# Kernel optimization log

Hardware: AMD Instinct MI355X
Metric: run time of the kernel (lower is better)

## Reference

```python
import jax, jax.numpy as jnp
import numpy as np

N1, E1 = 500_000, 4_000_000   # g_list[1]: path-complex graph
N0, E0 = 200_000, 1_000_000   # g_list[0]; E0 == 2*N1 (repeat-by-2 glue)
D_RBF = 64
GAMMA = 0.1


def rbf_map(x, W, b):
    # sklearn RBFSampler random Fourier features: sqrt(2/D) * cos(x @ W + b)
    return jnp.sqrt(2.0 / D_RBF) * jnp.cos(x @ W + b)


def gat_conv(x, W, al, ar, b, src, dst, num_nodes):
    # DGL GATConv: gather -> LeakyReLU edge attention -> per-dst softmax -> scatter-sum
    H, F = al.shape
    h = (x @ W).reshape(-1, H, F)                 # [N, H, F]
    el = jnp.sum(h * al, axis=-1)                 # [N, H]
    er = jnp.sum(h * ar, axis=-1)                 # [N, H]
    e = jax.nn.leaky_relu(el[src] + er[dst], 0.2) # [E, H]
    emax = jax.ops.segment_max(e, dst, num_segments=num_nodes)
    emax = jnp.where(jnp.isfinite(emax), emax, 0.0)
    a = jnp.exp(e - emax[dst])                    # [E, H]
    denom = jax.ops.segment_sum(a, dst, num_segments=num_nodes)          # [N, H]
    num = jax.ops.segment_sum(a[:, :, None] * h[src], dst, num_segments=num_nodes)  # [N, H, F]
    return num / jnp.maximum(denom, 1e-9)[:, :, None] + b.reshape(1, H, F)


def setup_inputs() -> dict:
    key = jax.random.key(0)
    ks = jax.random.split(key, 32)
    s = 0.1
    inp = {
        'feat1': jax.random.normal(ks[0], (N1, 2), jnp.float32),
        'src1': jax.random.randint(ks[1], (E1,), 0, N1, jnp.int32),
        'dst1': jax.random.randint(ks[2], (E1,), 0, N1, jnp.int32),
        'feat0': jax.random.normal(ks[3], (N0, 62), jnp.float32),
        'src0': jax.random.randint(ks[4], (E0,), 0, N0, jnp.int32),
        'dst0': jax.random.randint(ks[5], (E0,), 0, N0, jnp.int32),
        'edge_feat0': jax.random.normal(ks[6], (E0, 1), jnp.float32),
        'W_rbf1': jax.random.normal(ks[7], (2, D_RBF), jnp.float32) * np.sqrt(2.0 * GAMMA),
        'b_rbf1': jax.random.uniform(ks[8], (D_RBF,), jnp.float32) * (2.0 * np.pi),
        'W_rbf0': jax.random.normal(ks[9], (62, D_RBF), jnp.float32) * np.sqrt(2.0 * GAMMA),
        'b_rbf0': jax.random.uniform(ks[10], (D_RBF,), jnp.float32) * (2.0 * np.pi),
        'g1c1_W': jax.random.normal(ks[11], (64, 16), jnp.float32) * s,
        'g1c1_al': jax.random.normal(ks[12], (2, 8), jnp.float32) * s,
        'g1c1_ar': jax.random.normal(ks[13], (2, 8), jnp.float32) * s,
        'g1c1_b': jnp.zeros((16,), jnp.float32),
        'g1c2_W': jax.random.normal(ks[14], (16, 1), jnp.float32) * s,
        'g1c2_al': jax.random.normal(ks[15], (1, 1), jnp.float32) * s,
        'g1c2_ar': jax.random.normal(ks[16], (1, 1), jnp.float32) * s,
        'g1c2_b': jnp.zeros((1,), jnp.float32),
        'g2c1_W': jax.random.normal(ks[17], (64, 16), jnp.float32) * s,
        'g2c1_al': jax.random.normal(ks[18], (2, 8), jnp.float32) * s,
        'g2c1_ar': jax.random.normal(ks[19], (2, 8), jnp.float32) * s,
        'g2c1_b': jnp.zeros((16,), jnp.float32),
        'g2c2_W': jax.random.normal(ks[20], (16, 64), jnp.float32) * s,
        'g2c2_al': jax.random.normal(ks[21], (1, 64), jnp.float32) * s,
        'g2c2_ar': jax.random.normal(ks[22], (1, 64), jnp.float32) * s,
        'g2c2_b': jnp.zeros((64,), jnp.float32),
        'fc1_w': jax.random.normal(ks[23], (16, 64), jnp.float32) * s,
        'fc1_b': jnp.zeros((16,), jnp.float32),
        'out_w': jax.random.normal(ks[24], (1, 16), jnp.float32) * s,
        'out_b': jnp.zeros((1,), jnp.float32),
    }
    return inp


def reference(feat1, src1, dst1, feat0, src0, dst0, edge_feat0,
              W_rbf1, b_rbf1, W_rbf0, b_rbf0,
              g1c1_W, g1c1_al, g1c1_ar, g1c1_b,
              g1c2_W, g1c2_al, g1c2_ar, g1c2_b,
              g2c1_W, g2c1_al, g2c1_ar, g2c1_b,
              g2c2_W, g2c2_al, g2c2_ar, g2c2_b,
              fc1_w, fc1_b, out_w, out_b):
    # ---- branch on g_list[1] ----
    nf1 = rbf_map(feat1, W_rbf1, b_rbf1)                                  # [N1, 64]
    h1 = gat_conv(nf1, g1c1_W, g1c1_al, g1c1_ar, g1c1_b, src1, dst1, N1).reshape(N1, 16)
    h1 = jax.nn.relu(h1)
    out1 = gat_conv(h1, g1c2_W, g1c2_al, g1c2_ar, g1c2_b, src1, dst1, N1).reshape(N1, 1)
    # repeat-each-row-twice + add g0 edge feats (dead wrt final output: GATConv
    # has no .weight attr so initialize_weights is a no-op in the original too)
    ef = jnp.repeat(out1, 2, axis=0) + edge_feat0                         # [E0, 1]
    _ = ef
    # ---- branch on g_list[0] ----
    nf0 = rbf_map(feat0, W_rbf0, b_rbf0)                                  # [N0, 64]
    h0 = gat_conv(nf0, g2c1_W, g2c1_al, g2c1_ar, g2c1_b, src0, dst0, N0).reshape(N0, 16)
    h0 = jax.nn.relu(h0)
    out2 = gat_conv(h0, g2c2_W, g2c2_al, g2c2_ar, g2c2_b, src0, dst0, N0).reshape(N0, 64)
    # ---- dense tail ----
    h = jnp.mean(out2, axis=0, keepdims=True)                             # [1, 64]
    h = jax.nn.relu(h)                                                    # dropout: eval identity
    h = jax.nn.relu(h @ fc1_w.T + fc1_b)                                  # [1, 16]
    h = h @ out_w.T + out_b                                               # [1, 1]
    return jnp.squeeze(h, axis=1)                                         # [1]
```

## Files before the change

kernel.cpp:

```cpp
#include <hip/hip_runtime.h>
#include <math.h>


#define LRELU(v) ((v) > 0.0f ? (v) : 0.2f * (v))

__global__ __launch_bounds__(64) void k_prep(const float* __restrict__ W2,
                                             const float* __restrict__ al2,
                                             const float* __restrict__ ar2,
                                             float* __restrict__ wl,
                                             float* __restrict__ wr) {
    int i = threadIdx.x;
    if (i >= 16) return;
    float sl = 0.f, sr = 0.f;
    for (int f = 0; f < 64; ++f) {
        float w = W2[i * 64 + f];
        sl += w * al2[f];
        sr += w * ar2[f];
    }
    wl[i] = sl;
    wr[i] = sr;
}

__global__ __launch_bounds__(256) void k_rbf_proj(
    const float* __restrict__ feat0, const float* __restrict__ Wr,
    const float* __restrict__ br, const float* __restrict__ W1,
    const float* __restrict__ al1, const float* __restrict__ ar1,
    float* __restrict__ h1p, float* __restrict__ el1, float* __restrict__ er1,
    int N) {
    int n = blockIdx.x * blockDim.x + threadIdx.x;
    if (n >= N) return;

    float x[62];
    const float2* fp = reinterpret_cast<const float2*>(feat0 + (size_t)n * 62);
#pragma unroll
    for (int k = 0; k < 31; ++k) {
        float2 v = fp[k];
        x[2 * k] = v.x;
        x[2 * k + 1] = v.y;
    }

    float hp[16];
#pragma unroll
    for (int i = 0; i < 16; ++i) hp[i] = 0.f;

    const float cst = 0.17677669529663687f;
#pragma unroll 4
    for (int j = 0; j < 64; ++j) {
        float acc = br[j];
#pragma unroll
        for (int k = 0; k < 62; ++k) acc += x[k] * Wr[k * 64 + j];
        float nfj = cst * cosf(acc);
#pragma unroll
        for (int i = 0; i < 16; ++i) hp[i] += nfj * W1[j * 16 + i];
    }

    float e_l[2] = {0.f, 0.f}, e_r[2] = {0.f, 0.f};
#pragma unroll
    for (int i = 0; i < 16; ++i) {
        e_l[i >> 3] += hp[i] * al1[i];
        e_r[i >> 3] += hp[i] * ar1[i];
    }

    float4* ho = reinterpret_cast<float4*>(h1p + (size_t)n * 16);
    ho[0] = make_float4(hp[0], hp[1], hp[2], hp[3]);
    ho[1] = make_float4(hp[4], hp[5], hp[6], hp[7]);
    ho[2] = make_float4(hp[8], hp[9], hp[10], hp[11]);
    ho[3] = make_float4(hp[12], hp[13], hp[14], hp[15]);
    el1[n * 2 + 0] = e_l[0];
    el1[n * 2 + 1] = e_l[1];
    er1[n * 2 + 0] = e_r[0];
    er1[n * 2 + 1] = e_r[1];
}

__global__ __launch_bounds__(256) void k_edge1(
    const int* __restrict__ src, const int* __restrict__ dst,
    const float* __restrict__ el, const float* __restrict__ er,
    const float* __restrict__ hsrc, float* __restrict__ num,
    float* __restrict__ den, int E) {
    int tid = blockIdx.x * blockDim.x + threadIdx.x;
    int e = tid >> 4;
    if (e >= E) return;
    int t = tid & 15;
    int h = t >> 3;
    int s = src[e], d = dst[e];
    float v = el[s * 2 + h] + er[d * 2 + h];
    v = LRELU(v);
    float a = __expf(v);
    float hv = hsrc[(size_t)s * 16 + t];
    atomicAdd(&num[(size_t)d * 16 + t], a * hv);
    if ((t & 7) == 0) atomicAdd(&den[d * 2 + h], a);
}

__global__ __launch_bounds__(256) void k_fin1(
    const float* __restrict__ num, const float* __restrict__ den,
    const float* __restrict__ b1, const float* __restrict__ wl,
    const float* __restrict__ wr, float* __restrict__ h0,
    float* __restrict__ el2, float* __restrict__ er2, int N) {
    int n = blockIdx.x * blockDim.x + threadIdx.x;
    if (n >= N) return;
    float dn0 = fmaxf(den[n * 2 + 0], 1e-9f);
    float dn1 = fmaxf(den[n * 2 + 1], 1e-9f);
    const float4* np = reinterpret_cast<const float4*>(num + (size_t)n * 16);
    float q[16];
#pragma unroll
    for (int v4 = 0; v4 < 4; ++v4) {
        float4 nv = np[v4];
        q[v4 * 4 + 0] = nv.x;
        q[v4 * 4 + 1] = nv.y;
        q[v4 * 4 + 2] = nv.z;
        q[v4 * 4 + 3] = nv.w;
    }
    float sl = 0.f, sr = 0.f;
#pragma unroll
    for (int i = 0; i < 16; ++i) {
        float dn = (i < 8) ? dn0 : dn1;
        float val = q[i] / dn + b1[i];
        val = fmaxf(val, 0.f);
        q[i] = val;
        sl += val * wl[i];
        sr += val * wr[i];
    }
    float4* ho = reinterpret_cast<float4*>(h0 + (size_t)n * 16);
    ho[0] = make_float4(q[0], q[1], q[2], q[3]);
    ho[1] = make_float4(q[4], q[5], q[6], q[7]);
    ho[2] = make_float4(q[8], q[9], q[10], q[11]);
    ho[3] = make_float4(q[12], q[13], q[14], q[15]);
    el2[n] = sl;
    er2[n] = sr;
}

__global__ __launch_bounds__(256) void k_edge2(
    const int* __restrict__ src, const int* __restrict__ dst,
    const float* __restrict__ el, const float* __restrict__ er,
    const float* __restrict__ h0, float* __restrict__ num,
    float* __restrict__ den, int E) {
    int tid = blockIdx.x * blockDim.x + threadIdx.x;
    int e = tid >> 4;
    if (e >= E) return;
    int t = tid & 15;
    int s = src[e], d = dst[e];
    float v = el[s] + er[d];
    v = LRELU(v);
    float a = __expf(v);
    float hv = h0[(size_t)s * 16 + t];
    atomicAdd(&num[(size_t)d * 16 + t], a * hv);
    if (t == 0) atomicAdd(&den[d], a);
}

__global__ __launch_bounds__(256) void k_sum(const float* __restrict__ num,
                                             const float* __restrict__ den,
                                             float* __restrict__ s16, int N) {
    int tid = blockIdx.x * blockDim.x + threadIdx.x;
    int t = tid & 15;
    int g = tid >> 4;
    int ngrp = (gridDim.x * blockDim.x) >> 4;
    float acc = 0.f;
    for (int n = g; n < N; n += ngrp) {
        float dn = fmaxf(den[n], 1e-9f);
        acc += num[(size_t)n * 16 + t] / dn;
    }
    __shared__ float lds[256];
    lds[threadIdx.x] = acc;
    __syncthreads();
    if (threadIdx.x < 16) {
        float s = 0.f;
        for (int i = threadIdx.x; i < 256; i += 16) s += lds[i];
        atomicAdd(&s16[threadIdx.x], s);
    }
}

__global__ __launch_bounds__(64) void k_tail(
    const float* __restrict__ s16, const float* __restrict__ W2,
    const float* __restrict__ b2, const float* __restrict__ fc1w,
    const float* __restrict__ fc1b, const float* __restrict__ outw,
    const float* __restrict__ outb, float* __restrict__ out, float invN) {
    if (threadIdx.x != 0 || blockIdx.x != 0) return;
    float m[16];
#pragma unroll
    for (int i = 0; i < 16; ++i) m[i] = s16[i] * invN;
    float h16[16];
#pragma unroll
    for (int j = 0; j < 16; ++j) h16[j] = 0.f;
    for (int f = 0; f < 64; ++f) {
        float v = b2[f];
#pragma unroll
        for (int i = 0; i < 16; ++i) v += m[i] * W2[i * 64 + f];
        v = fmaxf(v, 0.f);
#pragma unroll
        for (int j = 0; j < 16; ++j) h16[j] += v * fc1w[j * 64 + f];
    }
    float o = outb[0];
#pragma unroll
    for (int j = 0; j < 16; ++j) {
        float t = fmaxf(h16[j] + fc1b[j], 0.f);
        o += t * outw[j];
    }
    out[0] = o;
}

extern "C" void kernel_launch(void* const* d_in, const int* in_sizes, int n_in,
                              void* d_out, int out_size, void* d_ws,
                              size_t ws_size, hipStream_t stream) {
    const float* feat0 = (const float*)d_in[3];
    const int* src0 = (const int*)d_in[4];
    const int* dst0 = (const int*)d_in[5];
    const float* Wr = (const float*)d_in[9];
    const float* br = (const float*)d_in[10];
    const float* W1 = (const float*)d_in[19];
    const float* al1 = (const float*)d_in[20];
    const float* ar1 = (const float*)d_in[21];
    const float* b1 = (const float*)d_in[22];
    const float* W2 = (const float*)d_in[23];
    const float* al2 = (const float*)d_in[24];
    const float* ar2 = (const float*)d_in[25];
    const float* b2 = (const float*)d_in[26];
    const float* fc1w = (const float*)d_in[27];
    const float* fc1b = (const float*)d_in[28];
    const float* outw = (const float*)d_in[29];
    const float* outb = (const float*)d_in[30];

    const int N = in_sizes[3] / 62;
    const int E = in_sizes[4];
    const size_t Nz = (size_t)N;

    float* ws = (float*)d_ws;
    float* num1 = ws;
    float* den1 = ws + 16 * Nz;
    float* num2 = ws + 18 * Nz;
    float* den2 = ws + 34 * Nz;
    float* s16 = ws + 35 * Nz;
    float* wl = ws + 35 * Nz + 16;
    float* wr = ws + 35 * Nz + 32;
    float* h1p = ws + 35 * Nz + 48;
    float* el1 = h1p + 16 * Nz;
    float* er1 = el1 + 2 * Nz;
    float* h0 = er1 + 2 * Nz;
    float* el2 = h0 + 16 * Nz;
    float* er2 = el2 + Nz;

    hipMemsetAsync(ws, 0, (35 * Nz + 16) * sizeof(float), stream);

    const int nb = (N + 255) / 256;
    const long long etot = (long long)E * 16;
    const int eb = (int)((etot + 255) / 256);

    k_prep<<<1, 64, 0, stream>>>(W2, al2, ar2, wl, wr);
    k_rbf_proj<<<nb, 256, 0, stream>>>(feat0, Wr, br, W1, al1, ar1, h1p, el1,
                                       er1, N);
    k_edge1<<<eb, 256, 0, stream>>>(src0, dst0, el1, er1, h1p, num1, den1, E);
    k_fin1<<<nb, 256, 0, stream>>>(num1, den1, b1, wl, wr, h0, el2, er2, N);
    k_edge2<<<eb, 256, 0, stream>>>(src0, dst0, el2, er2, h0, num2, den2, E);
    k_sum<<<256, 256, 0, stream>>>(num2, den2, s16, N);
    k_tail<<<1, 64, 0, stream>>>(s16, W2, b2, fc1w, fc1b, outw, outb,
                                 (float*)d_out, 1.0f / (float)N);
}
```

Before: 469.8 us.

## Build dst-sorted CSR on device and replace atomic edge scatter with per-node gather

Each call now builds a CSR by destination: a degree histogram, a three-kernel prefix scan and an atomic fill pass. The two GAT layers become gather kernels in which 16 lanes per destination node accumulate the numerator and denominator in registers. The finalize step and the node-mean reduction are fused into those kernels. This removes the 16 float atomics per edge and the large zeroing memset, at the cost of extra preprocessing launches and atomics on integer counters. Per-node loops now follow each node's in-degree, so work per group varies.

```diff
diff --git a/kernel.cpp b/kernel.cpp
--- a/kernel.cpp
+++ b/kernel.cpp
@@ -21,6 +21,77 @@
     wr[i] = sr;
 }
 
+__global__ __launch_bounds__(256) void k_hist(const int* __restrict__ dst,
+                                              int* __restrict__ deg, int E) {
+    int e = blockIdx.x * 256 + threadIdx.x;
+    if (e < E) atomicAdd(&deg[dst[e]], 1);
+}
+
+__global__ __launch_bounds__(1024) void k_scan1(const int* __restrict__ deg,
+                                                int* __restrict__ partial,
+                                                int N) {
+    __shared__ int lds[1024];
+    int i = blockIdx.x * 1024 + threadIdx.x;
+    lds[threadIdx.x] = (i < N) ? deg[i] : 0;
+    __syncthreads();
+    for (int s = 512; s > 0; s >>= 1) {
+        if (threadIdx.x < s) lds[threadIdx.x] += lds[threadIdx.x + s];
+        __syncthreads();
+    }
+    if (threadIdx.x == 0) partial[blockIdx.x] = lds[0];
+}
+
+__global__ __launch_bounds__(256) void k_scan2(const int* __restrict__ partial,
+                                               int* __restrict__ partoff,
+                                               int nb) {
+    __shared__ int lds[256];
+    int t = threadIdx.x;
+    int v = (t < nb) ? partial[t] : 0;
+    lds[t] = v;
+    __syncthreads();
+    for (int s = 1; s < 256; s <<= 1) {
+        int add = (t >= s) ? lds[t - s] : 0;
+        __syncthreads();
+        lds[t] += add;
+        __syncthreads();
+    }
+    if (t < nb) partoff[t] = lds[t] - v;
+}
+
+__global__ __launch_bounds__(1024) void k_scan3(const int* __restrict__ deg,
+                                                const int* __restrict__ partoff,
+                                                int* __restrict__ off,
+                                                int* __restrict__ cur, int N) {
+    __shared__ int lds[1024];
+    int t = threadIdx.x;
+    int i = blockIdx.x * 1024 + t;
+    int v = (i < N) ? deg[i] : 0;
+    lds[t] = v;
+    __syncthreads();
+    for (int s = 1; s < 1024; s <<= 1) {
+        int add = (t >= s) ? lds[t - s] : 0;
+        __syncthreads();
+        lds[t] += add;
+        __syncthreads();
+    }
+    if (i < N) {
+        int ex = lds[t] - v + partoff[blockIdx.x];
+        off[i] = ex;
+        cur[i] = ex;
+    }
+}
+
+__global__ __launch_bounds__(256) void k_fill(const int* __restrict__ src,
+                                              const int* __restrict__ dst,
+                                              int* __restrict__ cur,
+                                              int* __restrict__ csr, int E) {
+    int e = blockIdx.x * 256 + threadIdx.x;
+    if (e >= E) return;
+    int d = dst[e];
+    int pos = atomicAdd(&cur[d], 1);
+    csr[pos] = src[e];
+}
+
 __global__ __launch_bounds__(256) void k_rbf_proj(
     const float* __restrict__ feat0, const float* __restrict__ Wr,
     const float* __restrict__ br, const float* __restrict__ W1,
@@ -72,101 +143,67 @@
     er1[n * 2 + 1] = e_r[1];
 }
 
-__global__ __launch_bounds__(256) void k_edge1(
-    const int* __restrict__ src, const int* __restrict__ dst,
-    const float* __restrict__ el, const float* __restrict__ er,
-    const float* __restrict__ hsrc, float* __restrict__ num,
-    float* __restrict__ den, int E) {
-    int tid = blockIdx.x * blockDim.x + threadIdx.x;
-    int e = tid >> 4;
-    if (e >= E) return;
-    int t = tid & 15;
-    int h = t >> 3;
-    int s = src[e], d = dst[e];
-    float v = el[s * 2 + h] + er[d * 2 + h];
-    v = LRELU(v);
-    float a = __expf(v);
-    float hv = hsrc[(size_t)s * 16 + t];
-    atomicAdd(&num[(size_t)d * 16 + t], a * hv);
-    if ((t & 7) == 0) atomicAdd(&den[d * 2 + h], a);
-}
-
-__global__ __launch_bounds__(256) void k_fin1(
-    const float* __restrict__ num, const float* __restrict__ den,
+__global__ __launch_bounds__(256) void k_gat1(
+    const int* __restrict__ off, const int* __restrict__ deg,
+    const int* __restrict__ csr, const float* __restrict__ el1,
+    const float* __restrict__ er1, const float* __restrict__ h1p,
     const float* __restrict__ b1, const float* __restrict__ wl,
     const float* __restrict__ wr, float* __restrict__ h0,
     float* __restrict__ el2, float* __restrict__ er2, int N) {
-    int n = blockIdx.x * blockDim.x + threadIdx.x;
-    if (n >= N) return;
-    float dn0 = fmaxf(den[n * 2 + 0], 1e-9f);
-    float dn1 = fmaxf(den[n * 2 + 1], 1e-9f);
-    const float4* np = reinterpret_cast<const float4*>(num + (size_t)n * 16);
-    float q[16];
-#pragma unroll
-    for (int v4 = 0; v4 < 4; ++v4) {
-        float4 nv = np[v4];
-        q[v4 * 4 + 0] = nv.x;
-        q[v4 * 4 + 1] = nv.y;
-        q[v4 * 4 + 2] = nv.z;
-        q[v4 * 4 + 3] = nv.w;
-    }
-    float sl = 0.f, sr = 0.f;
-#pragma unroll
-    for (int i = 0; i < 16; ++i) {
-        float dn = (i < 8) ? dn0 : dn1;
-        float val = q[i] / dn + b1[i];
-        val = fmaxf(val, 0.f);
-        q[i] = val;
-        sl += val * wl[i];
-        sr += val * wr[i];
-    }
-    float4* ho = reinterpret_cast<float4*>(h0 + (size_t)n * 16);
-    ho[0] = make_float4(q[0], q[1], q[2], q[3]);
-    ho[1] = make_float4(q[4], q[5], q[6], q[7]);
-    ho[2] = make_float4(q[8], q[9], q[10], q[11]);
-    ho[3] = make_float4(q[12], q[13], q[14], q[15]);
-    el2[n] = sl;
-    er2[n] = sr;
-}
-
-__global__ __launch_bounds__(256) void k_edge2(
-    const int* __restrict__ src, const int* __restrict__ dst,
-    const float* __restrict__ el, const float* __restrict__ er,
-    const float* __restrict__ h0, float* __restrict__ num,
-    float* __restrict__ den, int E) {
-    int tid = blockIdx.x * blockDim.x + threadIdx.x;
-    int e = tid >> 4;
-    if (e >= E) return;
-    int t = tid & 15;
-    int s = src[e], d = dst[e];
-    float v = el[s] + er[d];
-    v = LRELU(v);
-    float a = __expf(v);
-    float hv = h0[(size_t)s * 16 + t];
-    atomicAdd(&num[(size_t)d * 16 + t], a * hv);
-    if (t == 0) atomicAdd(&den[d], a);
-}
-
-__global__ __launch_bounds__(256) void k_sum(const float* __restrict__ num,
-                                             const float* __restrict__ den,
-                                             float* __restrict__ s16, int N) {
-    int tid = blockIdx.x * blockDim.x + threadIdx.x;
-    int t = tid & 15;
-    int g = tid >> 4;
-    int ngrp = (gridDim.x * blockDim.x) >> 4;
-    float acc = 0.f;
-    for (int n = g; n < N; n += ngrp) {
-        float dn = fmaxf(den[n], 1e-9f);
-        acc += num[(size_t)n * 16 + t] / dn;
-    }
-    __shared__ float lds[256];
-    lds[threadIdx.x] = acc;
-    __syncthreads();
-    if (threadIdx.x < 16) {
-        float s = 0.f;
-        for (int i = threadIdx.x; i < 256; i += 16) s += lds[i];
-        atomicAdd(&s16[threadIdx.x], s);
-    }
+    int tid = blockIdx.x * 256 + threadIdx.x;
+    int d = tid >> 4;
+    if (d >= N) return;
+    int t = tid & 15, h = t >> 3;
+    float erd = er1[d * 2 + h];
+    int start = off[d], dg = deg[d];
+    float acc = 0.f, den = 0.f;
+    for (int j = 0; j < dg; ++j) {
+        int s = csr[start + j];
+        float a = __expf(LRELU(el1[s * 2 + h] + erd));
+        acc += a * h1p[(size_t)s * 16 + t];
+        den += a;
+    }
+    float val = fmaxf(acc / fmaxf(den, 1e-9f) + b1[t], 0.f);
+    h0[(size_t)d * 16 + t] = val;
+    float pl = val * wl[t], pr = val * wr[t];
+#pragma unroll
+    for (int m = 1; m < 16; m <<= 1) {
+        pl += __shfl_xor(pl, m);
+        pr += __shfl_xor(pr, m);
+    }
+    if (t == 0) {
+        el2[d] = pl;
+        er2[d] = pr;
+    }
+}
+
+__global__ __launch_bounds__(256) void k_gat2(
+    const int* __restrict__ off, const int* __restrict__ deg,
+    const int* __restrict__ csr, const float* __restrict__ el2,
+    const float* __restrict__ er2, const float* __restrict__ h0,
+    float* __restrict__ s16, int N) {
+    __shared__ float bsum[16];
+    if (threadIdx.x < 16) bsum[threadIdx.x] = 0.f;
+    __syncthreads();
+    int t = threadIdx.x & 15;
+    int g = (blockIdx.x * 256 + threadIdx.x) >> 4;
+    int ng = (gridDim.x * 256) >> 4;
+    float tot = 0.f;
+    for (int d = g; d < N; d += ng) {
+        float erd = er2[d];
+        int start = off[d], dg = deg[d];
+        float acc = 0.f, den = 0.f;
+        for (int j = 0; j < dg; ++j) {
+            int s = csr[start + j];
+            float a = __expf(LRELU(el2[s] + erd));
+            acc += a * h0[(size_t)s * 16 + t];
+            den += a;
+        }
+        tot += acc / fmaxf(den, 1e-9f);
+    }
+    atomicAdd(&bsum[t], tot);
+    __syncthreads();
+    if (threadIdx.x < 16) atomicAdd(&s16[threadIdx.x], bsum[threadIdx.x]);
 }
 
 __global__ __launch_bounds__(64) void k_tail(
@@ -223,34 +260,41 @@
     const int E = in_sizes[4];
     const size_t Nz = (size_t)N;
 
-    float* ws = (float*)d_ws;
-    float* num1 = ws;
-    float* den1 = ws + 16 * Nz;
-    float* num2 = ws + 18 * Nz;
-    float* den2 = ws + 34 * Nz;
-    float* s16 = ws + 35 * Nz;
-    float* wl = ws + 35 * Nz + 16;
-    float* wr = ws + 35 * Nz + 32;
-    float* h1p = ws + 35 * Nz + 48;
+    int* ws_i = (int*)d_ws;
+    float* ws_f = (float*)d_ws;
+    int* deg = ws_i;
+    float* s16 = ws_f + Nz;
+    int* off = ws_i + Nz + 16;
+    int* cur = ws_i + 2 * Nz + 16;
+    int* partial = ws_i + 3 * Nz + 16;
+    int* partoff = ws_i + 3 * Nz + 272;
+    int* csr = ws_i + 3 * Nz + 528;
+    float* h1p = ws_f + 3 * Nz + 528 + (size_t)E;
     float* el1 = h1p + 16 * Nz;
     float* er1 = el1 + 2 * Nz;
     float* h0 = er1 + 2 * Nz;
     float* el2 = h0 + 16 * Nz;
     float* er2 = el2 + Nz;
-
-    hipMemsetAsync(ws, 0, (35 * Nz + 16) * sizeof(float), stream);
-
-    const int nb = (N + 255) / 256;
-    const long long etot = (long long)E * 16;
-    const int eb = (int)((etot + 255) / 256);
+    float* wl = er2 + Nz;
+    float* wr = wl + 16;
+
+    hipMemsetAsync(deg, 0, (Nz + 16) * sizeof(float), stream);
+
+    const int nb_n = (N + 255) / 256;
+    const int nb_e = (E + 255) / 256;
+    const int nb_scan = (N + 1023) / 1024;
 
     k_prep<<<1, 64, 0, stream>>>(W2, al2, ar2, wl, wr);
-    k_rbf_proj<<<nb, 256, 0, stream>>>(feat0, Wr, br, W1, al1, ar1, h1p, el1,
-                                       er1, N);
-    k_edge1<<<eb, 256, 0, stream>>>(src0, dst0, el1, er1, h1p, num1, den1, E);
-    k_fin1<<<nb, 256, 0, stream>>>(num1, den1, b1, wl, wr, h0, el2, er2, N);
-    k_edge2<<<eb, 256, 0, stream>>>(src0, dst0, el2, er2, h0, num2, den2, E);
-    k_sum<<<256, 256, 0, stream>>>(num2, den2, s16, N);
+    k_hist<<<nb_e, 256, 0, stream>>>(dst0, deg, E);
+    k_scan1<<<nb_scan, 1024, 0, stream>>>(deg, partial, N);
+    k_scan2<<<1, 256, 0, stream>>>(partial, partoff, nb_scan);
+    k_scan3<<<nb_scan, 1024, 0, stream>>>(deg, partoff, off, cur, N);
+    k_fill<<<nb_e, 256, 0, stream>>>(src0, dst0, cur, csr, E);
+    k_rbf_proj<<<nb_n, 256, 0, stream>>>(feat0, Wr, br, W1, al1, ar1, h1p,
+                                         el1, er1, N);
+    k_gat1<<<(N * 16 + 255) / 256, 256, 0, stream>>>(
+        off, deg, csr, el1, er1, h1p, b1, wl, wr, h0, el2, er2, N);
+    k_gat2<<<1024, 256, 0, stream>>>(off, deg, csr, el2, er2, h0, s16, N);
     k_tail<<<1, 64, 0, stream>>>(s16, W2, b2, fc1w, fc1b, outw, outb,
                                  (float*)d_out, 1.0f / (float)N);
 }
```

New measurement: 473.0 us. About the same (+0.7%).

## Replace second-layer scatter with direct weighted sum and fuse zeroing into projection

Applied to the files above, without the earlier changes.

Layer two is now computed as a per-destination denominator pass followed by an edge pass. That edge pass accumulates a*h0[src]/den2[dst] straight into the 16-wide global sum, so the N×16 num2 scatter with per-element atomics and the separate k_sum reduction go away. The memset and k_prep are folded into the projection kernel, which also stages the RBF and W1 weights in LDS and splits the dot product across four accumulators. In exchange the edges are read twice and a division by den2 is done per edge, and summation order changes, which can alter floating-point results slightly.

```diff
diff --git a/kernel.cpp b/kernel.cpp
--- a/kernel.cpp
+++ b/kernel.cpp
@@ -3,31 +3,50 @@
 
 
 #define LRELU(v) ((v) > 0.0f ? (v) : 0.2f * (v))
-
-__global__ __launch_bounds__(64) void k_prep(const float* __restrict__ W2,
-                                             const float* __restrict__ al2,
-                                             const float* __restrict__ ar2,
-                                             float* __restrict__ wl,
-                                             float* __restrict__ wr) {
-    int i = threadIdx.x;
-    if (i >= 16) return;
-    float sl = 0.f, sr = 0.f;
-    for (int f = 0; f < 64; ++f) {
-        float w = W2[i * 64 + f];
-        sl += w * al2[f];
-        sr += w * ar2[f];
-    }
-    wl[i] = sl;
-    wr[i] = sr;
-}
 
 __global__ __launch_bounds__(256) void k_rbf_proj(
     const float* __restrict__ feat0, const float* __restrict__ Wr,
     const float* __restrict__ br, const float* __restrict__ W1,
     const float* __restrict__ al1, const float* __restrict__ ar1,
+    const float* __restrict__ W2, const float* __restrict__ al2,
+    const float* __restrict__ ar2, float* __restrict__ num1,
+    float* __restrict__ den1, float* __restrict__ den2,
+    float* __restrict__ s16, float* __restrict__ wl, float* __restrict__ wr,
     float* __restrict__ h1p, float* __restrict__ el1, float* __restrict__ er1,
     int N) {
-    int n = blockIdx.x * blockDim.x + threadIdx.x;
+    __shared__ float sWr[62 * 64];
+    __shared__ float sW1[64 * 16];
+    __shared__ float sbr[64];
+    __shared__ float sal[16], sar[16];
+
+    const int tid = threadIdx.x;
+    const int n = blockIdx.x * 256 + tid;
+
+    if (n < N) {
+        float4 z4 = make_float4(0.f, 0.f, 0.f, 0.f);
+        float4* np = reinterpret_cast<float4*>(num1 + (size_t)n * 16);
+        np[0] = z4; np[1] = z4; np[2] = z4; np[3] = z4;
+        *reinterpret_cast<float2*>(den1 + n * 2) = make_float2(0.f, 0.f);
+        den2[n] = 0.f;
+    }
+    if (blockIdx.x == 0 && tid < 16) {
+        s16[tid] = 0.f;
+        float sl = 0.f, sr = 0.f;
+        for (int f = 0; f < 64; ++f) {
+            float w = W2[tid * 64 + f];
+            sl += w * al2[f];
+            sr += w * ar2[f];
+        }
+        wl[tid] = sl;
+        wr[tid] = sr;
+    }
+
+    for (int i = tid; i < 62 * 64; i += 256) sWr[i] = Wr[i];
+    for (int i = tid; i < 64 * 16; i += 256) sW1[i] = W1[i];
+    if (tid < 64) sbr[tid] = br[tid];
+    if (tid < 16) { sal[tid] = al1[tid]; sar[tid] = ar1[tid]; }
+    __syncthreads();
+
     if (n >= N) return;
 
     float x[62];
@@ -44,21 +63,28 @@
     for (int i = 0; i < 16; ++i) hp[i] = 0.f;
 
     const float cst = 0.17677669529663687f;
-#pragma unroll 4
     for (int j = 0; j < 64; ++j) {
-        float acc = br[j];
-#pragma unroll
-        for (int k = 0; k < 62; ++k) acc += x[k] * Wr[k * 64 + j];
+        float a0 = 0.f, a1 = 0.f, a2 = 0.f, a3 = 0.f;
+#pragma unroll
+        for (int k = 0; k < 60; k += 4) {
+            a0 += x[k + 0] * sWr[(k + 0) * 64 + j];
+            a1 += x[k + 1] * sWr[(k + 1) * 64 + j];
+            a2 += x[k + 2] * sWr[(k + 2) * 64 + j];
+            a3 += x[k + 3] * sWr[(k + 3) * 64 + j];
+        }
+        a0 += x[60] * sWr[60 * 64 + j];
+        a1 += x[61] * sWr[61 * 64 + j];
+        float acc = sbr[j] + ((a0 + a1) + (a2 + a3));
         float nfj = cst * cosf(acc);
 #pragma unroll
-        for (int i = 0; i < 16; ++i) hp[i] += nfj * W1[j * 16 + i];
+        for (int i = 0; i < 16; ++i) hp[i] += nfj * sW1[j * 16 + i];
     }
 
     float e_l[2] = {0.f, 0.f}, e_r[2] = {0.f, 0.f};
 #pragma unroll
     for (int i = 0; i < 16; ++i) {
-        e_l[i >> 3] += hp[i] * al1[i];
-        e_r[i >> 3] += hp[i] * ar1[i];
+        e_l[i >> 3] += hp[i] * sal[i];
+        e_r[i >> 3] += hp[i] * sar[i];
     }
 
     float4* ho = reinterpret_cast<float4*>(h1p + (size_t)n * 16);
@@ -66,10 +92,8 @@
     ho[1] = make_float4(hp[4], hp[5], hp[6], hp[7]);
     ho[2] = make_float4(hp[8], hp[9], hp[10], hp[11]);
     ho[3] = make_float4(hp[12], hp[13], hp[14], hp[15]);
-    el1[n * 2 + 0] = e_l[0];
-    el1[n * 2 + 1] = e_l[1];
-    er1[n * 2 + 0] = e_r[0];
-    er1[n * 2 + 1] = e_r[1];
+    *reinterpret_cast<float2*>(el1 + n * 2) = make_float2(e_l[0], e_l[1]);
+    *reinterpret_cast<float2*>(er1 + n * 2) = make_float2(e_r[0], e_r[1]);
 }
 
 __global__ __launch_bounds__(256) void k_edge1(
@@ -77,7 +101,7 @@
     const float* __restrict__ el, const float* __restrict__ er,
     const float* __restrict__ hsrc, float* __restrict__ num,
     float* __restrict__ den, int E) {
-    int tid = blockIdx.x * blockDim.x + threadIdx.x;
+    int tid = blockIdx.x * 256 + threadIdx.x;
     int e = tid >> 4;
     if (e >= E) return;
     int t = tid & 15;
@@ -96,7 +120,7 @@
     const float* __restrict__ b1, const float* __restrict__ wl,
     const float* __restrict__ wr, float* __restrict__ h0,
     float* __restrict__ el2, float* __restrict__ er2, int N) {
-    int n = blockIdx.x * blockDim.x + threadIdx.x;
+    int n = blockIdx.x * 256 + threadIdx.x;
     if (n >= N) return;
     float dn0 = fmaxf(den[n * 2 + 0], 1e-9f);
     float dn1 = fmaxf(den[n * 2 + 1], 1e-9f);
@@ -114,8 +138,7 @@
 #pragma unroll
     for (int i = 0; i < 16; ++i) {
         float dn = (i < 8) ? dn0 : dn1;
-        float val = q[i] / dn + b1[i];
-        val = fmaxf(val, 0.f);
+        float val = fmaxf(q[i] / dn + b1[i], 0.f);
         q[i] = val;
         sl += val * wl[i];
         sr += val * wr[i];
@@ -129,44 +152,41 @@
     er2[n] = sr;
 }
 
-__global__ __launch_bounds__(256) void k_edge2(
+__global__ __launch_bounds__(256) void k_den2(
     const int* __restrict__ src, const int* __restrict__ dst,
-    const float* __restrict__ el, const float* __restrict__ er,
-    const float* __restrict__ h0, float* __restrict__ num,
-    float* __restrict__ den, int E) {
-    int tid = blockIdx.x * blockDim.x + threadIdx.x;
-    int e = tid >> 4;
+    const float* __restrict__ el2, const float* __restrict__ er2,
+    float* __restrict__ den2, int E) {
+    int e = blockIdx.x * 256 + threadIdx.x;
     if (e >= E) return;
-    int t = tid & 15;
-    int s = src[e], d = dst[e];
-    float v = el[s] + er[d];
+    float v = el2[src[e]] + er2[dst[e]];
     v = LRELU(v);
-    float a = __expf(v);
-    float hv = h0[(size_t)s * 16 + t];
-    atomicAdd(&num[(size_t)d * 16 + t], a * hv);
-    if (t == 0) atomicAdd(&den[d], a);
-}
-
-__global__ __launch_bounds__(256) void k_sum(const float* __restrict__ num,
-                                             const float* __restrict__ den,
-                                             float* __restrict__ s16, int N) {
-    int tid = blockIdx.x * blockDim.x + threadIdx.x;
-    int t = tid & 15;
-    int g = tid >> 4;
-    int ngrp = (gridDim.x * blockDim.x) >> 4;
-    float acc = 0.f;
-    for (int n = g; n < N; n += ngrp) {
-        float dn = fmaxf(den[n], 1e-9f);
-        acc += num[(size_t)n * 16 + t] / dn;
-    }
-    __shared__ float lds[256];
-    lds[threadIdx.x] = acc;
+    atomicAdd(&den2[dst[e]], __expf(v));
+}
+
+__global__ __launch_bounds__(256) void k_pv(
+    const int* __restrict__ src, const int* __restrict__ dst,
+    const float* __restrict__ el2, const float* __restrict__ er2,
+    const float* __restrict__ den2, const float* __restrict__ h0,
+    float* __restrict__ s16, int E) {
+    __shared__ float bsum[16];
+    if (threadIdx.x < 16) bsum[threadIdx.x] = 0.f;
     __syncthreads();
-    if (threadIdx.x < 16) {
-        float s = 0.f;
-        for (int i = threadIdx.x; i < 256; i += 16) s += lds[i];
-        atomicAdd(&s16[threadIdx.x], s);
-    }
+    int t = threadIdx.x & 15;
+    int g = (blockIdx.x * 256 + threadIdx.x) >> 4;
+    int ng = (gridDim.x * 256) >> 4;
+    float tot = 0.f;
+    for (int e = g; e < E; e += ng) {
+        int s = src[e], d = dst[e];
+        float v = el2[s] + er2[d];
+        v = LRELU(v);
+        float a = __expf(v);
+        tot += a * h0[(size_t)s * 16 + t] / den2[d];
+    }
+    tot += __shfl_xor(tot, 16);
+    tot += __shfl_xor(tot, 32);
+    if ((threadIdx.x & 63) < 16) atomicAdd(&bsum[t], tot);
+    __syncthreads();
+    if (threadIdx.x < 16) atomicAdd(&s16[threadIdx.x], bsum[threadIdx.x]);
 }
 
 __global__ __launch_bounds__(64) void k_tail(
@@ -192,8 +212,8 @@
     float o = outb[0];
 #pragma unroll
     for (int j = 0; j < 16; ++j) {
-        float t = fmaxf(h16[j] + fc1b[j], 0.f);
-        o += t * outw[j];
+        float tq = fmaxf(h16[j] + fc1b[j], 0.f);
+        o += tq * outw[j];
     }
     out[0] = o;
 }
@@ -226,31 +246,29 @@
     float* ws = (float*)d_ws;
     float* num1 = ws;
     float* den1 = ws + 16 * Nz;
-    float* num2 = ws + 18 * Nz;
-    float* den2 = ws + 34 * Nz;
-    float* s16 = ws + 35 * Nz;
-    float* wl = ws + 35 * Nz + 16;
-    float* wr = ws + 35 * Nz + 32;
-    float* h1p = ws + 35 * Nz + 48;
+    float* den2 = ws + 18 * Nz;
+    float* s16 = ws + 19 * Nz;
+    float* wl = ws + 19 * Nz + 16;
+    float* wr = ws + 19 * Nz + 32;
+    float* h1p = ws + 19 * Nz + 48;
     float* el1 = h1p + 16 * Nz;
     float* er1 = el1 + 2 * Nz;
     float* h0 = er1 + 2 * Nz;
     float* el2 = h0 + 16 * Nz;
     float* er2 = el2 + Nz;
 
-    hipMemsetAsync(ws, 0, (35 * Nz + 16) * sizeof(float), stream);
-
-    const int nb = (N + 255) / 256;
-    const long long etot = (long long)E * 16;
-    const int eb = (int)((etot + 255) / 256);
-
-    k_prep<<<1, 64, 0, stream>>>(W2, al2, ar2, wl, wr);
-    k_rbf_proj<<<nb, 256, 0, stream>>>(feat0, Wr, br, W1, al1, ar1, h1p, el1,
-                                       er1, N);
-    k_edge1<<<eb, 256, 0, stream>>>(src0, dst0, el1, er1, h1p, num1, den1, E);
-    k_fin1<<<nb, 256, 0, stream>>>(num1, den1, b1, wl, wr, h0, el2, er2, N);
-    k_edge2<<<eb, 256, 0, stream>>>(src0, dst0, el2, er2, h0, num2, den2, E);
-    k_sum<<<256, 256, 0, stream>>>(num2, den2, s16, N);
+    const int nb_n = (N + 255) / 256;
+    const int nb_e16 = (int)(((long long)E * 16 + 255) / 256);
+    const int nb_e = (E + 255) / 256;
+
+    k_rbf_proj<<<nb_n, 256, 0, stream>>>(feat0, Wr, br, W1, al1, ar1, W2, al2,
+                                         ar2, num1, den1, den2, s16, wl, wr,
+                                         h1p, el1, er1, N);
+    k_edge1<<<nb_e16, 256, 0, stream>>>(src0, dst0, el1, er1, h1p, num1, den1,
+                                        E);
+    k_fin1<<<nb_n, 256, 0, stream>>>(num1, den1, b1, wl, wr, h0, el2, er2, N);
+    k_den2<<<nb_e, 256, 0, stream>>>(src0, dst0, el2, er2, den2, E);
+    k_pv<<<2048, 256, 0, stream>>>(src0, dst0, el2, er2, den2, h0, s16, E);
     k_tail<<<1, 64, 0, stream>>>(s16, W2, b2, fc1w, fc1b, outw, outb,
                                  (float*)d_out, 1.0f / (float)N);
 }
```

Measured after the change: 471.8 us. Within noise of the previous version (+0.4%).
